# Kernel tuning notes

Hardware: AMD Instinct MI355X
Metric: run time of the kernel (lower is better)

## Reference

```python
import jax, jax.numpy as jnp
import numpy as np

NUM_USERS, NUM_ITEMS, NUM_REL = 100000, 50000, 8
EMB, LSTM_D, P, L = 64, 64, 100000, 4

def _linear_params(key, out_d, in_d):
    k1, k2 = jax.random.split(key)
    bound = 1.0 / np.sqrt(in_d)
    W = jax.random.uniform(k1, (out_d, in_d), jnp.float32, -bound, bound)
    b = jax.random.uniform(k2, (out_d,), jnp.float32, -bound, bound)
    return W, b

def setup_inputs() -> dict:
    key = jax.random.key(0)
    ks = jax.random.split(key, 16)
    inp = {
        'user_idx': jax.random.randint(ks[0], (1,), 0, NUM_USERS),
        'item_idx': jax.random.randint(ks[1], (1,), 0, NUM_ITEMS),
        'node_ids': jax.random.randint(ks[2], (P, L), 0, NUM_ITEMS),
        'node_types': jax.random.randint(ks[3], (P, L), 0, 2),
        'rel_idx': jax.random.randint(ks[4], (P, L), 0, NUM_REL),
        'user_emb': jax.random.normal(ks[5], (NUM_USERS, EMB), jnp.float32),
        'item_emb': jax.random.normal(ks[6], (NUM_ITEMS, EMB), jnp.float32),
        'relation_emb': jax.random.normal(ks[7], (NUM_REL, EMB), jnp.float32),
        'node_type_emb': jax.random.normal(ks[8], (2, EMB), jnp.float32),
    }
    # LSTM params (torch layout: gate order i, f, g, o; rows of size 4*lstm_dim)
    bound = 1.0 / np.sqrt(LSTM_D)
    kl = jax.random.split(ks[9], 4)
    inp['W_ih'] = jax.random.uniform(kl[0], (4 * LSTM_D, 3 * EMB), jnp.float32, -bound, bound)
    inp['W_hh'] = jax.random.uniform(kl[1], (4 * LSTM_D, LSTM_D), jnp.float32, -bound, bound)
    inp['b_ih'] = jax.random.uniform(kl[2], (4 * LSTM_D,), jnp.float32, -bound, bound)
    inp['b_hh'] = jax.random.uniform(kl[3], (4 * LSTM_D,), jnp.float32, -bound, bound)
    ka = jax.random.split(ks[10], 2)
    inp['att_W1'], inp['att_b1'] = _linear_params(ka[0], 128, LSTM_D + 2 * EMB)
    inp['att_W2'], inp['att_b2'] = _linear_params(ka[1], 1, 128)
    kv = jax.random.split(ks[11], 2)
    inp['val_W1'], inp['val_b1'] = _linear_params(kv[0], 32, LSTM_D)
    inp['val_W2'], inp['val_b2'] = _linear_params(kv[1], 1, 32)
    kd = jax.random.split(ks[12], 2)
    inp['adv_W1'], inp['adv_b1'] = _linear_params(kd[0], 32, LSTM_D)
    inp['adv_W2'], inp['adv_b2'] = _linear_params(kd[1], 1, 32)
    ksf = jax.random.split(ks[13], 2)
    inp['saf_W1'], inp['saf_b1'] = _linear_params(ksf[0], 32, 2 * EMB)
    inp['saf_W2'], inp['saf_b2'] = _linear_params(ksf[1], 1, 32)
    return inp

def _forward(user_idx, item_idx, node_ids, node_types, rel_idx,
             user_emb, item_emb, relation_emb, node_type_emb,
             W_ih, W_hh, b_ih, b_hh,
             att_W1, att_b1, att_W2, att_b2,
             val_W1, val_b1, val_W2, val_b2,
             adv_W1, adv_b1, adv_W2, adv_b2,
             saf_W1, saf_b1, saf_W2, saf_b2):
    u = user_emb[user_idx]  # [1, EMB]
    it = item_emb[item_idx]  # [1, EMB]
    # per-step embeddings, batched over all P paths at once  -> [P, L, EMB]
    node_e = jnp.where(node_types[..., None] == 0, user_emb[node_ids], item_emb[node_ids])
    type_e = node_type_emb[node_types]
    rel_e = relation_emb[rel_idx]
    feats = jnp.concatenate([node_e, type_e, rel_e], axis=-1)  # [P, L, 3*EMB]

    def lstm_step(carry, x_t):  # x_t: [P, 3*EMB]
        h, c = carry
        z = x_t @ W_ih.T + h @ W_hh.T + (b_ih + b_hh)  # [P, 4*LSTM_D]
        i_g, f_g, g_g, o_g = jnp.split(z, 4, axis=-1)
        i_g = jax.nn.sigmoid(i_g); f_g = jax.nn.sigmoid(f_g)
        g_g = jnp.tanh(g_g); o_g = jax.nn.sigmoid(o_g)
        c = f_g * c + i_g * g_g
        h = o_g * jnp.tanh(c)
        return (h, c), None

    h0 = jnp.zeros((node_ids.shape[0], LSTM_D), feats.dtype)
    (h_n, _), _ = jax.lax.scan(lstm_step, (h0, h0), feats.transpose(1, 0, 2))
    path_embs = h_n  # [P, LSTM_D]

    context = jnp.concatenate([u, it], axis=-1)  # [1, 2*EMB]
    ctx_rep = jnp.broadcast_to(context, (path_embs.shape[0], context.shape[1]))
    att_in = jnp.concatenate([path_embs, ctx_rep], axis=1)  # [P, LSTM_D+2*EMB]
    att_scores = jax.nn.relu(att_in @ att_W1.T + att_b1) @ att_W2.T + att_b2  # [P, 1]
    att_weights = jax.nn.softmax(att_scores, axis=0)
    aggregated = jnp.sum(att_weights * path_embs, axis=0)  # [LSTM_D]

    value = jax.nn.relu(aggregated @ val_W1.T + val_b1) @ val_W2.T + val_b2  # [1]
    advantage = jax.nn.relu(aggregated @ adv_W1.T + adv_b1) @ adv_W2.T + adv_b2  # [1]
    q_value = value + (advantage - jnp.mean(advantage))
    safety = jax.nn.sigmoid(jax.nn.relu(context @ saf_W1.T + saf_b1) @ saf_W2.T + saf_b2)  # [1,1]
    prediction = q_value * safety  # [1,1]
    return prediction, att_weights

def reference(user_idx, item_idx, node_ids, node_types, rel_idx,
              user_emb, item_emb, relation_emb, node_type_emb,
              W_ih, W_hh, b_ih, b_hh,
              att_W1, att_b1, att_W2, att_b2,
              val_W1, val_b1, val_W2, val_b2,
              adv_W1, adv_b1, adv_W2, adv_b2,
              saf_W1, saf_b1, saf_W2, saf_b2):
    return _forward(user_idx, item_idx, node_ids, node_types, rel_idx,
                    user_emb, item_emb, relation_emb, node_type_emb,
                    W_ih, W_hh, b_ih, b_hh,
                    att_W1, att_b1, att_W2, att_b2,
                    val_W1, val_b1, val_W2, val_b2,
                    adv_W1, adv_b1, adv_W2, adv_b2,
                    saf_W1, saf_b1, saf_W2, saf_b2)
```

## Files before the change

### kernel.cpp

```cpp
#include <hip/hip_runtime.h>
#include <math.h>

#define P_TOT 100000
#define BM    32
#define NBLK  3125

#define OFF_BIH   0
#define OFF_BHH   24576
#define OFF_BA    32768
#define OFF_BSUM  36864
#define OFF_CTXP  37120
#define OFF_MISC  37248
#define OFF_E     37264
#define OFF_PE    137264
#define OFF_PAGG  140392
#define OFF_P2E   340392
#define OFF_P2AGG 340456
#define OFF_TAB   356864
#define OFF_TU    (OFF_TAB)
#define OFF_TI    (OFF_TAB + 3200000)
#define OFF_TR    (OFF_TAB + 4800000)
#define OFF_TT    (OFF_TAB + 4800256)
#define WS_FAST_BYTES ((size_t)(OFF_TAB + 4800320) * 4)

#define AHB   49152
#define ESO   57344
#define PARTO 57472
#define LDS_BYTES 59520

#define LOG2E  1.442695041f
#define LOG2E2 2.885390082f

typedef short bf16x8 __attribute__((ext_vector_type(8)));
typedef float f32x4  __attribute__((ext_vector_type(4)));

#define MFMA16(a,b,c) __builtin_amdgcn_mfma_f32_16x16x32_bf16((a),(b),(c),0,0,0)

__device__ __forceinline__ unsigned short cvh(float v){
  unsigned int u = __float_as_uint(v);
  return (unsigned short)((u + 0x7fffu + ((u>>16)&1u)) >> 16);
}
__device__ __forceinline__ float fexp2(float x){
#if __has_builtin(__builtin_amdgcn_exp2f)
  return __builtin_amdgcn_exp2f(x);
#else
  return exp2f(x);
#endif
}
__device__ __forceinline__ float frcp(float x){
#if __has_builtin(__builtin_amdgcn_rcpf)
  return __builtin_amdgcn_rcpf(x);
#else
  return 1.f/x;
#endif
}
__device__ __forceinline__ float sigm2(float zp){ return frcp(1.f + fexp2(-zp)); }
__device__ __forceinline__ float tanh2(float zp){
  float e2 = fexp2(zp);
  return (e2 - 1.f) * frcp(e2 + 1.f);
}
__device__ __forceinline__ float tanh_c(float c){ return tanh2(c * LOG2E2); }
__device__ __forceinline__ float sigm_f(float x){ return 1.f/(1.f+__expf(-x)); }

__global__ __launch_bounds__(256) void kprep(
    const int* __restrict__ user_idx, const int* __restrict__ item_idx,
    const float* __restrict__ user_emb, const float* __restrict__ item_emb,
    const float* __restrict__ W_ih, const float* __restrict__ W_hh,
    const float* __restrict__ b_ih, const float* __restrict__ b_hh,
    const float* __restrict__ att_W1, const float* __restrict__ att_b1,
    const float* __restrict__ saf_W1, const float* __restrict__ saf_b1,
    const float* __restrict__ saf_W2, const float* __restrict__ saf_b2,
    float* __restrict__ ws)
{
  const int t = threadIdx.x;
  for (int fb = blockIdx.x; fb < 144; fb += gridDim.x){
    const float* src; int base, rowlen, kc; bool perm; int w=0, nt=0, ntg=0;
    if (fb < 96){ kc = fb>>4; int rem = fb&15; w = rem>>1; nt = rem&1; perm = true;
                  base = OFF_BIH + fb*256; src = W_ih; rowlen = 192; }
    else if (fb < 128){ int f2 = fb-96; kc = f2>>4; int rem = f2&15; w = rem>>1; nt = rem&1; perm = true;
                  base = OFF_BHH + f2*256; src = W_hh; rowlen = 64; }
    else { int f3 = fb-128; kc = f3>>3; ntg = f3&7; perm = false;
                  base = OFF_BA + f3*256; src = att_W1; rowlen = 192; }
    unsigned short* dst = (unsigned short*)(ws + base);
    for (int e = t; e < 512; e += 256){
      int l = e>>3, j = e&7;
      int c = l&15;
      int n = perm ? (nt*2 + (c>>3))*64 + w*8 + (c&7)
                   : ntg*16 + c;
      int k = kc*32 + (l>>4)*8 + j;
      float v = src[n*rowlen + k];
      if (perm) v *= ((n>>6)==2 ? LOG2E2 : LOG2E);
      dst[e] = cvh(v);
    }
  }
  if (blockIdx.x == 0){
    __shared__ float ctx[128];
    if (t < 256) ws[OFF_BSUM+t] = (b_ih[t] + b_hh[t]) * ((t>>6)==2 ? LOG2E2 : LOG2E);
    if (t < 64){
      ctx[t]    = user_emb[user_idx[0]*64 + t];
      ctx[64+t] = item_emb[item_idx[0]*64 + t];
    }
    __syncthreads();
    if (t < 128){
      float s = att_b1[t];
      for (int k=0;k<128;++k) s = fmaf(att_W1[t*192 + 64 + k], ctx[k], s);
      ws[OFF_CTXP + t] = s;
    }
    if (t < 32){
      float s = saf_b1[t];
      for (int k=0;k<128;++k) s = fmaf(saf_W1[t*128+k], ctx[k], s);
      s = fmaxf(s, 0.f);
      float v = s * saf_W2[t];
      v += __shfl_xor(v,1); v += __shfl_xor(v,2); v += __shfl_xor(v,4);
      v += __shfl_xor(v,8); v += __shfl_xor(v,16);
      if (t==0) ws[OFF_MISC+0] = 1.f/(1.f+expf(-(v + saf_b2[0])));
    }
  }
}

__global__ __launch_bounds__(256) void kconv(
    const float* __restrict__ user_emb, const float* __restrict__ item_emb,
    const float* __restrict__ relation_emb, const float* __restrict__ node_type_emb,
    float* __restrict__ ws)
{
  const int gid = blockIdx.x*256 + threadIdx.x;
  const int row = gid >> 3, seg = gid & 7;
  if (row >= 150010) return;
  const float* src; int dstoff;
  if (row < 100000){ src = user_emb + row*64;             dstoff = OFF_TU + row*32; }
  else if (row < 150000){ src = item_emb + (row-100000)*64; dstoff = OFF_TI + (row-100000)*32; }
  else if (row < 150008){ src = relation_emb + (row-150000)*64; dstoff = OFF_TR + (row-150000)*32; }
  else { src = node_type_emb + (row-150008)*64;           dstoff = OFF_TT + (row-150008)*32; }
  float4 v0 = ((const float4*)(src + seg*8))[0];
  float4 v1 = ((const float4*)(src + seg*8))[1];
  uint4 hq;
  hq.x = (unsigned)cvh(v0.x) | ((unsigned)cvh(v0.y)<<16);
  hq.y = (unsigned)cvh(v0.z) | ((unsigned)cvh(v0.w)<<16);
  hq.z = (unsigned)cvh(v1.x) | ((unsigned)cvh(v1.y)<<16);
  hq.w = (unsigned)cvh(v1.z) | ((unsigned)cvh(v1.w)<<16);
  *(uint4*)((char*)(ws + dstoff) + seg*16) = hq;
}

template<int PRE>
__global__ __launch_bounds__(512,4) void klstm(
    const int* __restrict__ node_ids, const int* __restrict__ node_types,
    const int* __restrict__ rel_idx,
    const float* __restrict__ user_emb, const float* __restrict__ item_emb,
    const float* __restrict__ relation_emb, const float* __restrict__ node_type_emb,
    const float* __restrict__ att_W2, const float* __restrict__ att_b2,
    float* __restrict__ ws)
{
  __shared__ __align__(16) unsigned char smem[LDS_BYTES];
  const int t   = threadIdx.x;
  const int l   = t & 63, wid = t >> 6;
  const int ln  = l & 15, lk = l >> 4;
  const int bid = blockIdx.x, p0 = bid*BM;
  const bf16x8* Bih = (const bf16x8*)(ws + OFF_BIH);
  const bf16x8* Bhh = (const bf16x8*)(ws + OFF_BHH);
  const bf16x8* Bab = (const bf16x8*)(ws + OFF_BA);
  const int swA = (ln&7)<<4;

  {
    const int c8 = t&7, rr = t>>3;
    #pragma unroll
    for (int i=0;i<6;++i){
      int task = rr + i*64;
      int src = task>>7, s = (task>>5)&3, p = task&31;
      int gi = (p0+p)*4 + s;
      int dsta = (s*32 + p)*384 + ((src*128 + c8*16) ^ ((p&7)<<4));
      if (PRE){
        const char* rp;
        if (src==0){ int nid = node_ids[gi];
                     rp = (const char*)(ws + (node_types[gi]==0 ? OFF_TU + nid*32 : OFF_TI + nid*32)); }
        else if (src==1){ rp = (const char*)(ws + OFF_TT + node_types[gi]*32); }
        else { rp = (const char*)(ws + OFF_TR + rel_idx[gi]*32); }
        *(uint4*)(smem + dsta) = *(const uint4*)(rp + c8*16);
      } else {
        const float* sp;
        if (src==0){ int nid = node_ids[gi]; sp = (node_types[gi]==0 ? user_emb : item_emb) + nid*64; }
        else if (src==1){ sp = node_type_emb + node_types[gi]*64; }
        else { sp = relation_emb + rel_idx[gi]*64; }
        float4 v0 = ((const float4*)sp)[c8*2];
        float4 v1 = ((const float4*)sp)[c8*2+1];
        uint4 hq;
        hq.x = (unsigned)cvh(v0.x) | ((unsigned)cvh(v0.y)<<16);
        hq.y = (unsigned)cvh(v0.z) | ((unsigned)cvh(v0.w)<<16);
        hq.z = (unsigned)cvh(v1.x) | ((unsigned)cvh(v1.y)<<16);
        hq.w = (unsigned)cvh(v1.z) | ((unsigned)cvh(v1.w)<<16);
        *(uint4*)(smem + dsta) = hq;
      }
    }
  }
  f32x4 acc[4][2][2];
  {
    float bv0 = ws[OFF_BSUM + ((ln>>3))*64   + wid*8 + (ln&7)];
    float bv1 = ws[OFF_BSUM + (2+(ln>>3))*64 + wid*8 + (ln&7)];
    #pragma unroll
    for (int s=0;s<4;++s)
      #pragma unroll
      for (int pt=0;pt<2;++pt){
        acc[s][pt][0] = (f32x4){bv0,bv0,bv0,bv0};
        acc[s][pt][1] = (f32x4){bv1,bv1,bv1,bv1};
      }
  }
  __syncthreads();

  #pragma unroll 2
  for (int kc=0;kc<6;++kc){
    bf16x8 bh0 = Bih[(unsigned)((kc*16 + wid*2+0)*64 + l)];
    bf16x8 bh1 = Bih[(unsigned)((kc*16 + wid*2+1)*64 + l)];
    #pragma unroll
    for (int s=0;s<4;++s)
      #pragma unroll
      for (int pt=0;pt<2;++pt){
        bf16x8 ah = *(const bf16x8*)(smem + (s*32 + pt*16 + ln)*384 + ((kc*64 + lk*16) ^ swA));
        acc[s][pt][0] = MFMA16(ah, bh0, acc[s][pt][0]);
        acc[s][pt][1] = MFMA16(ah, bh1, acc[s][pt][1]);
      }
  }

  const int hi8 = ln>>3;
  const int dd  = wid*8 + (ln&7);
  float c0[2] = {0.f,0.f}, c1[2] = {0.f,0.f};
  #pragma unroll
  for (int s=0;s<4;++s){
    if (s > 0){
      const int rb = AHB + (s&1)*4096;
      #pragma unroll
      for (int kc=0;kc<2;++kc){
        bf16x8 bh0 = Bhh[(unsigned)((kc*16 + wid*2+0)*64 + l)];
        bf16x8 bh1 = Bhh[(unsigned)((kc*16 + wid*2+1)*64 + l)];
        #pragma unroll
        for (int pt=0;pt<2;++pt){
          bf16x8 ah = *(const bf16x8*)(smem + rb + (pt*16 + ln)*128 + ((kc*64 + lk*16) ^ swA));
          acc[s][pt][0] = MFMA16(ah, bh0, acc[s][pt][0]);
          acc[s][pt][1] = MFMA16(ah, bh1, acc[s][pt][1]);
        }
      }
    }
    const int wb = AHB + ((s&1)^1)*4096;
    #pragma unroll
    for (int pt=0;pt<2;++pt){
      float a00 = acc[s][pt][0][0], a01 = acc[s][pt][0][1], a02 = acc[s][pt][0][2], a03 = acc[s][pt][0][3];
      float a10 = acc[s][pt][1][0], a11 = acc[s][pt][1][1], a12 = acc[s][pt][1][2], a13 = acc[s][pt][1][3];
      float p00 = __shfl_xor(a00,8), p01 = __shfl_xor(a01,8);
      float p02 = __shfl_xor(a02,8), p03 = __shfl_xor(a03,8);
      float p10 = __shfl_xor(a10,8), p11 = __shfl_xor(a11,8);
      float p12 = __shfl_xor(a12,8), p13 = __shfl_xor(a13,8);
      float vi0 = hi8 ? p02 : a00;  float vf0 = hi8 ? a02 : p00;
      float vg0 = hi8 ? p12 : a10;  float vo0 = hi8 ? a12 : p10;
      float vi1 = hi8 ? p03 : a01;  float vf1 = hi8 ? a03 : p01;
      float vg1 = hi8 ? p13 : a11;  float vo1 = hi8 ? a13 : p11;
      float i0 = sigm2(vi0), f0 = sigm2(vf0), g0 = tanh2(vg0), o0 = sigm2(vo0);
      float i1 = sigm2(vi1), f1 = sigm2(vf1), g1 = tanh2(vg1), o1 = sigm2(vo1);
      c0[pt] = fmaf(f0, c0[pt], i0*g0);
      c1[pt] = fmaf(f1, c1[pt], i1*g1);
      float h0 = o0 * tanh_c(c0[pt]);
      float h1 = o1 * tanh_c(c1[pt]);
      int pth0 = pt*16 + lk*4 + hi8*2, pth1 = pth0 + 1;
      *(unsigned short*)(smem + wb + pth0*128 + ((dd*2) ^ ((pth0&7)<<4))) = cvh(h0);
      *(unsigned short*)(smem + wb + pth1*128 + ((dd*2) ^ ((pth1&7)<<4))) = cvh(h1);
    }
    __syncthreads();
  }

  {
    const int pt = wid>>2, wg = wid&3;
    f32x4 acc2[2];
    #pragma unroll
    for (int nt=0;nt<2;++nt){
      float cv = ws[OFF_CTXP + wg*32 + nt*16 + ln];
      acc2[nt] = (f32x4){cv,cv,cv,cv};
    }
    #pragma unroll
    for (int kc=0;kc<2;++kc){
      bf16x8 ah = *(const bf16x8*)(smem + AHB + (pt*16 + ln)*128 + ((kc*64 + lk*16) ^ swA));
      bf16x8 bh0 = Bab[(unsigned)((kc*8 + wg*2+0)*64 + l)];
      bf16x8 bh1 = Bab[(unsigned)((kc*8 + wg*2+1)*64 + l)];
      acc2[0] = MFMA16(ah, bh0, acc2[0]);
      acc2[1] = MFMA16(ah, bh1, acc2[1]);
    }
    __syncthreads();
    #pragma unroll
    for (int nt=0;nt<2;++nt)
      #pragma unroll
      for (int r=0;r<4;++r)
        *(float*)(smem + (pt*16 + lk*4+r)*512 + (wg*32 + nt*16 + ln)*4) = fmaxf(acc2[nt][r], 0.f);
  }
  __syncthreads();
  {
    int p = t>>4, seg = t&15;
    float4 a0 = *(const float4*)(smem + p*512 + seg*32);
    float4 a1 = *(const float4*)(smem + p*512 + seg*32 + 16);
    float4 w0 = *(const float4*)(att_W2 + seg*8);
    float4 w1 = *(const float4*)(att_W2 + seg*8 + 4);
    float sc = a0.x*w0.x; sc = fmaf(a0.y,w0.y,sc); sc = fmaf(a0.z,w0.z,sc); sc = fmaf(a0.w,w0.w,sc);
    sc = fmaf(a1.x,w1.x,sc); sc = fmaf(a1.y,w1.y,sc); sc = fmaf(a1.z,w1.z,sc); sc = fmaf(a1.w,w1.w,sc);
    sc += __shfl_xor(sc,1); sc += __shfl_xor(sc,2); sc += __shfl_xor(sc,4); sc += __shfl_xor(sc,8);
    if (seg == 0){
      float e = __expf(sc + att_b2[0]);
      *(float*)(smem + ESO + p*4) = e;
      ws[OFF_E + p0 + p] = e;
    }
  }
  __syncthreads();
  {
    int pg = t>>6, d = t&63;
    const float* es = (const float*)(smem + ESO);
    float a = 0.f;
    #pragma unroll
    for (int pi=0;pi<4;++pi){
      int p = pg*4 + pi;
      unsigned short hu = *(const unsigned short*)(smem + AHB + p*128 + ((d*2) ^ ((p&7)<<4)));
      a = fmaf(es[p], __uint_as_float((unsigned)hu << 16), a);
    }
    *(float*)(smem + PARTO + (pg*64+d)*4) = a;
  }
  __syncthreads();
  if (t < 64){
    const float* part = (const float*)(smem + PARTO);
    float a = 0.f;
    #pragma unroll
    for (int pg=0;pg<8;++pg) a += part[pg*64 + t];
    ws[OFF_PAGG + bid*64 + t] = a;
  }
  if (t < 32){
    float e2 = *(const float*)(smem + ESO + t*4);
    e2 += __shfl_xor(e2,1); e2 += __shfl_xor(e2,2);
    e2 += __shfl_xor(e2,4); e2 += __shfl_xor(e2,8); e2 += __shfl_xor(e2,16);
    if (t==0) ws[OFF_PE + bid] = e2;
  }
}

__global__ __launch_bounds__(256) void kredA(float* __restrict__ ws)
{
  const float* p_e   = ws + OFF_PE;
  const float* p_agg = ws + OFF_PAGG;
  __shared__ float red[256];
  const int b = blockIdx.x, t = threadIdx.x;
  const int s = b*4 + (t>>6), d = t&63;
  float a = 0.f;
  for (int row = s; row < NBLK; row += 256) a += p_agg[row*64 + d];
  ws[OFF_P2AGG + s*64 + d] = a;
  float pe = 0.f;
  {
    int i = b*49 + t;
    if (t < 49 && i < NBLK) pe = p_e[i];
  }
  pe += __shfl_xor(pe,1); pe += __shfl_xor(pe,2); pe += __shfl_xor(pe,4);
  pe += __shfl_xor(pe,8); pe += __shfl_xor(pe,16); pe += __shfl_xor(pe,32);
  if ((t&63)==0) red[t>>6] = pe;
  __syncthreads();
  if (t==0) ws[OFF_P2E + b] = red[0]+red[1]+red[2]+red[3];
}

__global__ __launch_bounds__(256) void kredB(
    const float* __restrict__ val_W1, const float* __restrict__ val_b1,
    const float* __restrict__ val_W2, const float* __restrict__ val_b2,
    float* __restrict__ ws, float* __restrict__ d_out)
{
  __shared__ float aggL[64];
  __shared__ float red[256];
  __shared__ float Zs;
  const int t = threadIdx.x;
  {
    float pe = (t < 64) ? ws[OFF_P2E + t] : 0.f;
    pe += __shfl_xor(pe,1); pe += __shfl_xor(pe,2); pe += __shfl_xor(pe,4);
    pe += __shfl_xor(pe,8); pe += __shfl_xor(pe,16); pe += __shfl_xor(pe,32);
    if (t==0){ Zs = pe; ws[OFF_MISC+1] = 1.f/pe; }
  }
  {
    int d = t&63, q = t>>6;
    float a = 0.f;
    #pragma unroll 4
    for (int s2=q; s2<256; s2+=4) a += ws[OFF_P2AGG + s2*64 + d];
    red[t] = a;
  }
  __syncthreads();
  if (t < 64) aggL[t] = (red[t] + red[64+t] + red[128+t] + red[192+t]) / Zs;
  __syncthreads();
  if (t < 32){
    float hv = val_b1[t];
    for (int k=0;k<64;++k) hv = fmaf(aggL[k], val_W1[t*64+k], hv);
    hv = fmaxf(hv, 0.f);
    float v = hv * val_W2[t];
    v += __shfl_xor(v,1); v += __shfl_xor(v,2); v += __shfl_xor(v,4);
    v += __shfl_xor(v,8); v += __shfl_xor(v,16);
    if (t==0) d_out[0] = (v + val_b2[0]) * ws[OFF_MISC+0];
  }
}

__global__ __launch_bounds__(256) void kweights(
    const float* __restrict__ ws, float* __restrict__ d_out)
{
  int p = blockIdx.x*256 + threadIdx.x;
  if (p < P_TOT) d_out[1+p] = ws[OFF_E + p] * ws[OFF_MISC+1];
}

extern "C" void kernel_launch(void* const* d_in, const int* in_sizes, int n_in,
                              void* d_out, int out_size, void* d_ws, size_t ws_size,
                              hipStream_t stream) {
  const int*   user_idx   = (const int*)  d_in[0];
  const int*   item_idx   = (const int*)  d_in[1];
  const int*   node_ids   = (const int*)  d_in[2];
  const int*   node_types = (const int*)  d_in[3];
  const int*   rel_idx    = (const int*)  d_in[4];
  const float* user_emb   = (const float*)d_in[5];
  const float* item_emb   = (const float*)d_in[6];
  const float* rel_emb    = (const float*)d_in[7];
  const float* ntype_emb  = (const float*)d_in[8];
  const float* W_ih       = (const float*)d_in[9];
  const float* W_hh       = (const float*)d_in[10];
  const float* b_ih       = (const float*)d_in[11];
  const float* b_hh       = (const float*)d_in[12];
  const float* att_W1     = (const float*)d_in[13];
  const float* att_b1     = (const float*)d_in[14];
  const float* att_W2     = (const float*)d_in[15];
  const float* att_b2     = (const float*)d_in[16];
  const float* val_W1     = (const float*)d_in[17];
  const float* val_b1     = (const float*)d_in[18];
  const float* val_W2     = (const float*)d_in[19];
  const float* val_b2     = (const float*)d_in[20];
  const float* saf_W1     = (const float*)d_in[25];
  const float* saf_b1     = (const float*)d_in[26];
  const float* saf_W2     = (const float*)d_in[27];
  const float* saf_b2     = (const float*)d_in[28];
  float* ws  = (float*)d_ws;
  float* out = (float*)d_out;

  const bool fast = (ws_size >= WS_FAST_BYTES);

  hipLaunchKernelGGL(kprep, dim3(64), dim3(256), 0, stream,
                     user_idx, item_idx, user_emb, item_emb,
                     W_ih, W_hh, b_ih, b_hh, att_W1, att_b1,
                     saf_W1, saf_b1, saf_W2, saf_b2, ws);
  if (fast){
    hipLaunchKernelGGL(kconv, dim3((150010*8+255)/256), dim3(256), 0, stream,
                       user_emb, item_emb, rel_emb, ntype_emb, ws);
    hipLaunchKernelGGL(klstm<1>, dim3(NBLK), dim3(512), 0, stream,
                       node_ids, node_types, rel_idx,
                       user_emb, item_emb, rel_emb, ntype_emb,
                       att_W2, att_b2, ws);
  } else {
    hipLaunchKernelGGL(klstm<0>, dim3(NBLK), dim3(512), 0, stream,
                       node_ids, node_types, rel_idx,
                       user_emb, item_emb, rel_emb, ntype_emb,
                       att_W2, att_b2, ws);
  }
  hipLaunchKernelGGL(kredA, dim3(64), dim3(256), 0, stream, ws);
  hipLaunchKernelGGL(kredB, dim3(1), dim3(256), 0, stream,
                     val_W1, val_b1, val_W2, val_b2, ws, out);
  hipLaunchKernelGGL(kweights, dim3((P_TOT+255)/256), dim3(256), 0, stream,
                     ws, out);
}
```

Before: 118.7 us.

## Gather inputs in two halves and compute input projection per step

The embedding gather into shared memory now happens in two halves (steps 0-1, then steps 2-3) instead of all four steps at once. This shrinks the shared-memory footprint from about 59KB to about 35KB. The input-projection MFMAs move inside the recurrent step loop, so the accumulators are per step (16 floats) instead of for all four steps (64 floats). The aim is lower register and LDS pressure and higher occupancy. The cost is an extra barrier and a mid-loop gather stall at step 2.

```diff
diff --git a/kernel.cpp b/kernel.cpp
--- a/kernel.cpp
+++ b/kernel.cpp
@@ -23,10 +23,10 @@
 #define OFF_TT    (OFF_TAB + 4800256)
 #define WS_FAST_BYTES ((size_t)(OFF_TAB + 4800320) * 4)
 
-#define AHB   49152
-#define ESO   57344
-#define PARTO 57472
-#define LDS_BYTES 59520
+#define AHB   24576
+#define ESO   32768
+#define PARTO 32896
+#define LDS_BYTES 34944
 
 #define LOG2E  1.442695041f
 #define LOG2E2 2.885390082f
@@ -60,7 +60,6 @@
   return (e2 - 1.f) * frcp(e2 + 1.f);
 }
 __device__ __forceinline__ float tanh_c(float c){ return tanh2(c * LOG2E2); }
-__device__ __forceinline__ float sigm_f(float x){ return 1.f/(1.f+__expf(-x)); }
 
 __global__ __launch_bounds__(256) void kprep(
     const int* __restrict__ user_idx, const int* __restrict__ item_idx,
@@ -159,15 +158,15 @@
   const bf16x8* Bhh = (const bf16x8*)(ws + OFF_BHH);
   const bf16x8* Bab = (const bf16x8*)(ws + OFF_BA);
   const int swA = (ln&7)<<4;
-
-  {
-    const int c8 = t&7, rr = t>>3;
-    #pragma unroll
-    for (int i=0;i<6;++i){
+  const int c8 = t&7, rr = t>>3;
+
+  auto gather_half = [&](int half){
+    #pragma unroll
+    for (int i=0;i<3;++i){
       int task = rr + i*64;
-      int src = task>>7, s = (task>>5)&3, p = task&31;
-      int gi = (p0+p)*4 + s;
-      int dsta = (s*32 + p)*384 + ((src*128 + c8*16) ^ ((p&7)<<4));
+      int src = task>>6, s2 = (task>>5)&1, p = task&31;
+      int gi = (p0+p)*4 + half*2 + s2;
+      int dsta = (s2*32 + p)*384 + ((src*128 + c8*16) ^ ((p&7)<<4));
       if (PRE){
         const char* rp;
         if (src==0){ int nid = node_ids[gi];
@@ -190,40 +189,41 @@
         *(uint4*)(smem + dsta) = hq;
       }
     }
-  }
-  f32x4 acc[4][2][2];
-  {
-    float bv0 = ws[OFF_BSUM + ((ln>>3))*64   + wid*8 + (ln&7)];
-    float bv1 = ws[OFF_BSUM + (2+(ln>>3))*64 + wid*8 + (ln&7)];
-    #pragma unroll
-    for (int s=0;s<4;++s)
-      #pragma unroll
-      for (int pt=0;pt<2;++pt){
-        acc[s][pt][0] = (f32x4){bv0,bv0,bv0,bv0};
-        acc[s][pt][1] = (f32x4){bv1,bv1,bv1,bv1};
-      }
-  }
-  __syncthreads();
-
-  #pragma unroll 2
-  for (int kc=0;kc<6;++kc){
-    bf16x8 bh0 = Bih[(unsigned)((kc*16 + wid*2+0)*64 + l)];
-    bf16x8 bh1 = Bih[(unsigned)((kc*16 + wid*2+1)*64 + l)];
-    #pragma unroll
-    for (int s=0;s<4;++s)
-      #pragma unroll
-      for (int pt=0;pt<2;++pt){
-        bf16x8 ah = *(const bf16x8*)(smem + (s*32 + pt*16 + ln)*384 + ((kc*64 + lk*16) ^ swA));
-        acc[s][pt][0] = MFMA16(ah, bh0, acc[s][pt][0]);
-        acc[s][pt][1] = MFMA16(ah, bh1, acc[s][pt][1]);
-      }
-  }
-
+  };
+
+  const float bv0 = ws[OFF_BSUM + ((ln>>3))*64   + wid*8 + (ln&7)];
+  const float bv1 = ws[OFF_BSUM + (2+(ln>>3))*64 + wid*8 + (ln&7)];
   const int hi8 = ln>>3;
   const int dd  = wid*8 + (ln&7);
   float c0[2] = {0.f,0.f}, c1[2] = {0.f,0.f};
+
+  gather_half(0);
+  __syncthreads();
+
   #pragma unroll
   for (int s=0;s<4;++s){
+    if (s == 2){
+      gather_half(1);
+      __syncthreads();
+    }
+    const int slot = s&1;
+    f32x4 acc[2][2];
+    #pragma unroll
+    for (int pt=0;pt<2;++pt){
+      acc[pt][0] = (f32x4){bv0,bv0,bv0,bv0};
+      acc[pt][1] = (f32x4){bv1,bv1,bv1,bv1};
+    }
+    #pragma unroll 2
+    for (int kc=0;kc<6;++kc){
+      bf16x8 bh0 = Bih[(unsigned)((kc*16 + wid*2+0)*64 + l)];
+      bf16x8 bh1 = Bih[(unsigned)((kc*16 + wid*2+1)*64 + l)];
+      #pragma unroll
+      for (int pt=0;pt<2;++pt){
+        bf16x8 ah = *(const bf16x8*)(smem + (slot*32 + pt*16 + ln)*384 + ((kc*64 + lk*16) ^ swA));
+        acc[pt][0] = MFMA16(ah, bh0, acc[pt][0]);
+        acc[pt][1] = MFMA16(ah, bh1, acc[pt][1]);
+      }
+    }
     if (s > 0){
       const int rb = AHB + (s&1)*4096;
       #pragma unroll
@@ -233,16 +233,16 @@
         #pragma unroll
         for (int pt=0;pt<2;++pt){
           bf16x8 ah = *(const bf16x8*)(smem + rb + (pt*16 + ln)*128 + ((kc*64 + lk*16) ^ swA));
-          acc[s][pt][0] = MFMA16(ah, bh0, acc[s][pt][0]);
-          acc[s][pt][1] = MFMA16(ah, bh1, acc[s][pt][1]);
+          acc[pt][0] = MFMA16(ah, bh0, acc[pt][0]);
+          acc[pt][1] = MFMA16(ah, bh1, acc[pt][1]);
         }
       }
     }
     const int wb = AHB + ((s&1)^1)*4096;
     #pragma unroll
     for (int pt=0;pt<2;++pt){
-      float a00 = acc[s][pt][0][0], a01 = acc[s][pt][0][1], a02 = acc[s][pt][0][2], a03 = acc[s][pt][0][3];
-      float a10 = acc[s][pt][1][0], a11 = acc[s][pt][1][1], a12 = acc[s][pt][1][2], a13 = acc[s][pt][1][3];
+      float a00 = acc[pt][0][0], a01 = acc[pt][0][1], a02 = acc[pt][0][2], a03 = acc[pt][0][3];
+      float a10 = acc[pt][1][0], a11 = acc[pt][1][1], a12 = acc[pt][1][2], a13 = acc[pt][1][3];
       float p00 = __shfl_xor(a00,8), p01 = __shfl_xor(a01,8);
       float p02 = __shfl_xor(a02,8), p03 = __shfl_xor(a03,8);
       float p10 = __shfl_xor(a10,8), p11 = __shfl_xor(a11,8);
```

New measurement: 127.6 us. +7.4%, slower.
